# Optimization experiments

Hardware: AMD Instinct MI355X
Metric: run time of the kernel (lower is better)

Reference implementation:

```python
import jax, jax.numpy as jnp
import numpy as np

B, T, D, H = 4, 2048, 1024, 16
HD = D // H  # 64

def setup_inputs() -> dict:
    key = jax.random.key(0)
    ks = jax.random.split(key, 6)
    s = 0.02
    x = jax.random.normal(ks[0], (B, T, D), dtype=jnp.float32)
    # per-head projection weights, torch Linear layout [out=HD, in=D], stacked over heads
    Wq = jax.random.normal(ks[1], (H, HD, D), dtype=jnp.float32) * s
    Wk = jax.random.normal(ks[2], (H, HD, D), dtype=jnp.float32) * s
    Wv = jax.random.normal(ks[3], (H, HD, D), dtype=jnp.float32) * s
    Wo = jax.random.normal(ks[4], (D, D), dtype=jnp.float32) * s
    bo = jax.random.normal(ks[5], (D,), dtype=jnp.float32) * s
    return {"x": x, "Wq": Wq, "Wk": Wk, "Wv": Wv, "Wo": Wo, "bo": bo}

def reference(x, Wq, Wk, Wv, Wo, bo):
    # per-head projections (same math as per-head nn.Linear, vectorized over heads)
    Q = jnp.einsum('btd,hkd->bhtk', x, Wq)
    K = jnp.einsum('bsd,hkd->bhsk', x, Wk)
    V = jnp.einsum('bsd,hkd->bhsk', x, Wv)
    scale = 1.0 / jnp.sqrt(jnp.asarray(HD, x.dtype))
    logits = jnp.einsum('bhtk,bhsk->bhts', Q, K) * scale  # [B,H,T,S]
    w = jax.nn.softmax(logits, axis=-1)
    out = jnp.einsum('bhts,bhsk->bhtk', w, V)  # [B,H,T,HD]
    # concat heads in order -> [B,T,D]
    cat = jnp.transpose(out, (0, 2, 1, 3)).reshape(B, T, D)
    return cat @ Wo.T + bo
```

## Files before the change

kernel.cpp:

```cpp
#include <hip/hip_runtime.h>
#include <hip/hip_bf16.h>
#include <stdint.h>
#include <math.h>

typedef unsigned short u16;
typedef uint32_t u32;
typedef __bf16 bf16x8 __attribute__((ext_vector_type(8)));
typedef float f32x4 __attribute__((ext_vector_type(4)));
typedef float f32x16 __attribute__((ext_vector_type(16)));
typedef u16 u16x8 __attribute__((ext_vector_type(8)));
typedef u16 u16x4 __attribute__((ext_vector_type(4)));

#define B_ 4
#define T_ 2048
#define D_ 1024
#define H_ 16
#define HD_ 64
#define M_ (B_*T_)
#define LDA 72

__device__ __forceinline__ u16 f2bf(float f) {
    union { __bf16 h; u16 u; } c;
    c.h = (__bf16)f;
    return c.u;
}

__device__ __forceinline__ void gl16(const u16* g, u16* l) {
    __builtin_amdgcn_global_load_lds(
        (__attribute__((address_space(1))) void*)g,
        (__attribute__((address_space(3))) void*)l, 16, 0, 0);
}

__device__ __forceinline__ f32x4 mfma16(bf16x8 a, bf16x8 b, f32x4 c) {
    return __builtin_amdgcn_mfma_f32_16x16x32_bf16(a, b, c, 0, 0, 0);
}

__device__ __forceinline__ f32x16 mfma32(bf16x8 a, bf16x8 b, f32x16 c) {
    return __builtin_amdgcn_mfma_f32_32x32x16_bf16(a, b, c, 0, 0, 0);
}

__device__ __forceinline__ u32 cvtpk_bf16(float lo, float hi) {
    u32 r;
    asm("v_cvt_pk_bf16_f32 %0, %1, %2" : "=v"(r) : "v"(lo), "v"(hi));
    return r;
}

__device__ __forceinline__ float fexp2(float x) {
    return __builtin_amdgcn_exp2f(x);
}

__global__ __launch_bounds__(256) void precast(
    const float* __restrict__ x,  const float* __restrict__ wq,
    const float* __restrict__ wk, const float* __restrict__ wv,
    const float* __restrict__ wo,
    u16* __restrict__ xb, u16* __restrict__ wqb, u16* __restrict__ wkb,
    u16* __restrict__ wvb, u16* __restrict__ wob)
{
    const int which = blockIdx.y;
    const float* src; u16* dst; int n;
    switch (which) {
        case 0: src = x;  dst = xb;  n = M_ * D_;  break;
        case 1: src = wq; dst = wqb; n = D_ * D_;  break;
        case 2: src = wk; dst = wkb; n = D_ * D_;  break;
        case 3: src = wv; dst = wvb; n = D_ * D_;  break;
        default: src = wo; dst = wob; n = D_ * D_; break;
    }
    int i = (blockIdx.x * 256 + threadIdx.x) * 4;
    if (i >= n) return;
    float4 v = *(const float4*)&src[i];
    u16x4 p = { f2bf(v.x), f2bf(v.y), f2bf(v.z), f2bf(v.w) };
    *(u16x4*)&dst[i] = p;
}

__device__ __forceinline__ void gemm_pipe(
    const u16* __restrict__ Xg, const u16* __restrict__ Wg,
    u16* AsBase, u16* BsBase,
    const int tid, const int wm, const int wn, const int l15, const int quad,
    f32x4 acc[8][4])
{
    const int swz = (quad ^ ((l15 >> 1) & 3)) * 8;

#pragma unroll
    for (int tt = 0; tt < 2; ++tt) {
#pragma unroll
        for (int i = 0; i < 4; ++i) {
            int c = tid + i * 256;
            int r = c >> 2, xs = (c & 3) ^ ((r >> 1) & 3);
            gl16(Xg + (size_t)r * 1024 + tt * 32 + xs * 8, AsBase + tt * 8192 + c * 8);
        }
#pragma unroll
        for (int i = 0; i < 2; ++i) {
            int c = tid + i * 256;
            int r = c >> 2, xs = (c & 3) ^ ((r >> 1) & 3);
            gl16(Wg + (size_t)r * 1024 + tt * 32 + xs * 8, BsBase + tt * 4096 + c * 8);
        }
    }

    for (int t = 0; t < 32; ++t) {
        if (t < 31) asm volatile("s_waitcnt vmcnt(6)" ::: "memory");
        else        asm volatile("s_waitcnt vmcnt(0)" ::: "memory");
        __builtin_amdgcn_s_barrier();
        __builtin_amdgcn_sched_barrier(0);
        const u16* Ac = AsBase + (t & 1) * 8192;
        const u16* Bc = BsBase + (t & 1) * 4096;
        bf16x8 af[8], bfr[4];
#pragma unroll
        for (int mf = 0; mf < 8; ++mf)
            af[mf] = *(const bf16x8*)&Ac[(wm * 128 + mf * 16 + l15) * 32 + swz];
#pragma unroll
        for (int nf = 0; nf < 4; ++nf)
            bfr[nf] = *(const bf16x8*)&Bc[(wn * 64 + nf * 16 + l15) * 32 + swz];
        asm volatile("s_waitcnt lgkmcnt(0)" ::: "memory");
        __builtin_amdgcn_sched_barrier(0);
        __builtin_amdgcn_s_barrier();
        if (t + 2 < 32) {
            const int k0 = (t + 2) * 32;
#pragma unroll
            for (int i = 0; i < 4; ++i) {
                int c = tid + i * 256;
                int r = c >> 2, xs = (c & 3) ^ ((r >> 1) & 3);
                gl16(Xg + (size_t)r * 1024 + k0 + xs * 8, AsBase + (t & 1) * 8192 + c * 8);
            }
#pragma unroll
            for (int i = 0; i < 2; ++i) {
                int c = tid + i * 256;
                int r = c >> 2, xs = (c & 3) ^ ((r >> 1) & 3);
                gl16(Wg + (size_t)r * 1024 + k0 + xs * 8, BsBase + (t & 1) * 4096 + c * 8);
            }
        }
        __builtin_amdgcn_s_setprio(1);
#pragma unroll
        for (int mf = 0; mf < 8; ++mf)
#pragma unroll
            for (int nf = 0; nf < 4; ++nf)
                acc[mf][nf] = mfma16(af[mf], bfr[nf], acc[mf][nf]);
        __builtin_amdgcn_s_setprio(0);
    }
}

__global__ __launch_bounds__(256, 2) void qkv_gemm(
    const u16* __restrict__ Xb, const u16* __restrict__ W3,
    u16* __restrict__ Qo, u16* __restrict__ Ko, u16* __restrict__ Vo)
{
    __shared__ __attribute__((aligned(16))) u16 As[2][256 * 32];
    __shared__ __attribute__((aligned(16))) u16 Bs[2][128 * 32];

    const int wg = blockIdx.x + 24 * blockIdx.y;
    const int xcd = wg & 7, k = wg >> 3;
    const int by = xcd + 8 * (k / 24);
    const int bx = k % 24;
    const int n0 = bx * 128, m0 = by * 256;
    const u16* Xg = Xb + (size_t)m0 * 1024;
    const u16* Wg = W3 + (size_t)n0 * 1024;
    const int z = n0 >> 10;
    u16* Out = (z == 0) ? Qo : (z == 1) ? Ko : Vo;
    const float qs = (z == 0) ? 0.125f * 1.44269504088896340736f : 1.0f;

    const int tid = threadIdx.x;
    const int lane = tid & 63;
    const int wave = tid >> 6;
    const int wm = wave >> 1, wn = wave & 1;
    const int l15 = lane & 15, quad = lane >> 4;

    f32x4 acc[8][4];
#pragma unroll
    for (int i = 0; i < 8; ++i)
#pragma unroll
        for (int j = 0; j < 4; ++j) acc[i][j] = (f32x4){0.f, 0.f, 0.f, 0.f};

    gemm_pipe(Xg, Wg, &As[0][0], &Bs[0][0], tid, wm, wn, l15, quad, acc);

#pragma unroll
    for (int mf = 0; mf < 8; ++mf)
#pragma unroll
        for (int nf = 0; nf < 4; ++nf)
#pragma unroll
            for (int r = 0; r < 4; ++r) {
                int row = m0 + wm * 128 + mf * 16 + quad * 4 + r;
                int colz = (n0 & 1023) + wn * 64 + nf * 16 + l15;
                int b = row >> 11;
                int t = row & 2047;
                int h = colz >> 6;
                int hd = colz & 63;
                Out[((b * H_ + h) * T_ + t) * HD_ + hd] = f2bf(acc[mf][nf][r] * qs);
            }
}

__global__ __launch_bounds__(256, 2) void out_gemm(
    const u16* __restrict__ Xb, const u16* __restrict__ W3,
    const float* __restrict__ bias, float* __restrict__ Out)
{
    __shared__ __attribute__((aligned(16))) u16 As[2][256 * 32];
    __shared__ __attribute__((aligned(16))) u16 Bs[2][128 * 32];

    const int wg = blockIdx.x + 8 * blockIdx.y;
    const int xcd = wg & 7, k = wg >> 3;
    const int by = xcd + 8 * (k >> 3);
    const int bx = k & 7;
    const int n0 = bx * 128, m0 = by * 256;
    const u16* Xg = Xb + (size_t)m0 * 1024;
    const u16* Wg = W3 + (size_t)n0 * 1024;

    const int tid = threadIdx.x;
    const int lane = tid & 63;
    const int wave = tid >> 6;
    const int wm = wave >> 1, wn = wave & 1;
    const int l15 = lane & 15, quad = lane >> 4;

    f32x4 acc[8][4];
#pragma unroll
    for (int i = 0; i < 8; ++i)
#pragma unroll
        for (int j = 0; j < 4; ++j) acc[i][j] = (f32x4){0.f, 0.f, 0.f, 0.f};

    gemm_pipe(Xg, Wg, &As[0][0], &Bs[0][0], tid, wm, wn, l15, quad, acc);

#pragma unroll
    for (int mf = 0; mf < 8; ++mf)
#pragma unroll
        for (int nf = 0; nf < 4; ++nf)
#pragma unroll
            for (int r = 0; r < 4; ++r) {
                int row = m0 + wm * 128 + mf * 16 + quad * 4 + r;
                int col = n0 + wn * 64 + nf * 16 + l15;
                Out[(size_t)row * 1024 + col] = acc[mf][nf][r] + bias[col];
            }
}

__global__ __launch_bounds__(256) void vtrans(
    const u16* __restrict__ Vin, u16* __restrict__ Vout)
{
    __shared__ __attribute__((aligned(16))) u16 Tt[64 * LDA];
    const int tid = threadIdx.x;
    const int t0 = blockIdx.x * 64;
    const size_t base = (size_t)blockIdx.y * T_ * HD_;

#pragma unroll
    for (int i = 0; i < 2; ++i) {
        int ch = tid + i * 256;
        int r = ch >> 3, c = (ch & 7) * 8;
        u16x8 v = *(const u16x8*)&Vin[base + (size_t)(t0 + r) * HD_ + c];
#pragma unroll
        for (int j = 0; j < 8; ++j) {
            int hd = c + j;
            int blk = (r >> 3) ^ ((hd >> 3) & 7);
            Tt[hd * LDA + blk * 8 + (r & 7)] = v[j];
        }
    }
    __syncthreads();
#pragma unroll
    for (int i = 0; i < 2; ++i) {
        int ch = tid + i * 256;
        int hd = ch >> 3, n = ch & 7;
        int k = (hd >> 3) & 7;
        u16x8 v = *(const u16x8*)&Tt[hd * LDA + ((n ^ k) * 8)];
        *(u16x8*)&Vout[base + (size_t)hd * T_ + t0 + n * 8] = v;
    }
}

__global__ __launch_bounds__(256, 2) void attn(
    const u16* __restrict__ Q, const u16* __restrict__ K,
    const u16* __restrict__ Vt_g, u16* __restrict__ O)
{
    __shared__ __attribute__((aligned(16))) u16 Ks[2 * 4096];
    __shared__ __attribute__((aligned(16))) u16 Vts[2 * 4096];
    __shared__ float lps[4 * 64];

    const int tid = threadIdx.x;
    const int lane = tid & 63, w = tid >> 6;
    const int l31 = lane & 31, hi = lane >> 5;

    const int wg = blockIdx.x + (T_ / 256) * (blockIdx.y + H_ * blockIdx.z);
    const int xcd = wg & 7, k8 = wg >> 3;
    const int bh = xcd + 8 * (k8 >> 3);
    const int xq = k8 & 7;
    const int b = bh >> 4, h = bh & 15;
    const int t0 = xq * 256 + w * 64;

    const size_t base = (size_t)bh * T_ * HD_;
    const u16* Kb = K + base;
    const u16* Vtb = Vt_g + base;
    const u16* Qb = Q + base + (size_t)t0 * HD_;

    const int ca = tid,        ra = ca >> 3,  sa = (ca & 7) ^ (ra & 7);
    const int cb2 = tid + 256, rb = cb2 >> 3, sb = (cb2 & 7) ^ (rb & 7);
    const u16* kpa = Kb  + (size_t)ra * 64 + sa * 8;
    const u16* kpb = Kb  + (size_t)rb * 64 + sb * 8;
    const u16* vpa = Vtb + (size_t)ra * T_ + sa * 8;
    const u16* vpb = Vtb + (size_t)rb * T_ + sb * 8;

    int foff[2][4];
#pragma unroll
    for (int nt = 0; nt < 2; ++nt) {
        const int row = nt * 32 + l31;
#pragma unroll
        for (int kb = 0; kb < 4; ++kb)
            foff[nt][kb] = row * 64 + (((kb * 2 + hi) ^ (row & 7)) * 8);
    }

    bf16x8 qf[2][4];
#pragma unroll
    for (int qt = 0; qt < 2; ++qt)
#pragma unroll
        for (int kb = 0; kb < 4; ++kb)
            qf[qt][kb] = *(const bf16x8*)&Qb[(qt * 32 + l31) * 64 + kb * 16 + hi * 8];

    f32x16 zacc;
#pragma unroll
    for (int i = 0; i < 16; ++i) zacc[i] = 0.f;
    f32x16 oacc[2][2];
#pragma unroll
    for (int qt = 0; qt < 2; ++qt)
#pragma unroll
        for (int cb = 0; cb < 2; ++cb) oacc[qt][cb] = zacc;
    float lp[2] = {0.f, 0.f};

    gl16(kpa, &Ks[ca * 8]);
    gl16(kpb, &Ks[cb2 * 8]);
    gl16(vpa, &Vts[ca * 8]);
    gl16(vpb, &Vts[cb2 * 8]);
    asm volatile("s_waitcnt vmcnt(0)" ::: "memory");
    __syncthreads();

    int buf = 0;
    for (int s0 = 0; s0 < T_; s0 += 64) {
        if (s0 + 64 < T_) {
            const int nb = buf ^ 1;
            const size_t ko = (size_t)(s0 + 64) * 64;
            const size_t vo = (size_t)(s0 + 64);
            gl16(kpa + ko, &Ks[nb * 4096 + ca * 8]);
            gl16(kpb + ko, &Ks[nb * 4096 + cb2 * 8]);
            gl16(vpa + vo, &Vts[nb * 4096 + ca * 8]);
            gl16(vpb + vo, &Vts[nb * 4096 + cb2 * 8]);
        }
        const u16* Kc = &Ks[buf * 4096];
        const u16* Vc = &Vts[buf * 4096];

        bf16x8 pa[2][4];
#pragma unroll
        for (int nt = 0; nt < 2; ++nt) {
            bf16x8 kf[4];
#pragma unroll
            for (int kb = 0; kb < 4; ++kb)
                kf[kb] = *(const bf16x8*)&Kc[foff[nt][kb]];
#pragma unroll
            for (int qt = 0; qt < 2; ++qt) {
                __builtin_amdgcn_s_setprio(1);
                f32x16 sacc = mfma32(kf[0], qf[qt][0], zacc);
                sacc = mfma32(kf[1], qf[qt][1], sacc);
                sacc = mfma32(kf[2], qf[qt][2], sacc);
                sacc = mfma32(kf[3], qf[qt][3], sacc);
                __builtin_amdgcn_s_setprio(0);
                float p[16];
#pragma unroll
                for (int r = 0; r < 16; ++r) p[r] = fexp2(sacc[r]);
                float s01 = (p[0] + p[1]) + (p[2] + p[3]);
                float s23 = (p[4] + p[5]) + (p[6] + p[7]);
                float s45 = (p[8] + p[9]) + (p[10] + p[11]);
                float s67 = (p[12] + p[13]) + (p[14] + p[15]);
                lp[qt] += (s01 + s23) + (s45 + s67);
#pragma unroll
                for (int c = 0; c < 2; ++c) {
                    const int g = c * 8;
                    u32 a0 = cvtpk_bf16(p[g + 0], p[g + 1]);
                    u32 a1 = cvtpk_bf16(p[g + 2], p[g + 3]);
                    u32 b0 = cvtpk_bf16(p[g + 4], p[g + 5]);
                    u32 b1 = cvtpk_bf16(p[g + 6], p[g + 7]);
                    asm("v_permlane32_swap_b32 %0, %1" : "+v"(a0), "+v"(b0));
                    asm("v_permlane32_swap_b32 %0, %1" : "+v"(a1), "+v"(b1));
                    union { u32 wq[4]; bf16x8 v; } uu;
                    uu.wq[0] = a0; uu.wq[1] = a1; uu.wq[2] = b0; uu.wq[3] = b1;
                    pa[qt][nt * 2 + c] = uu.v;
                }
            }
        }
        __builtin_amdgcn_s_setprio(1);
#pragma unroll
        for (int cb = 0; cb < 2; ++cb)
#pragma unroll
            for (int kb = 0; kb < 4; ++kb) {
                bf16x8 vf = *(const bf16x8*)&Vc[foff[cb][kb]];
                oacc[0][cb] = mfma32(pa[0][kb], vf, oacc[0][cb]);
                oacc[1][cb] = mfma32(pa[1][kb], vf, oacc[1][cb]);
            }
        __builtin_amdgcn_s_setprio(0);
        asm volatile("s_waitcnt vmcnt(0)" ::: "memory");
        __syncthreads();
        buf ^= 1;
    }

#pragma unroll
    for (int qt = 0; qt < 2; ++qt) {
        lp[qt] += __shfl_xor(lp[qt], 32);
        lps[w * 64 + qt * 32 + l31] = lp[qt];
    }
    asm volatile("s_waitcnt lgkmcnt(0)" ::: "memory");

#pragma unroll
    for (int qt = 0; qt < 2; ++qt)
#pragma unroll
        for (int r = 0; r < 16; ++r) {
            const int trow = (r & 3) + 8 * (r >> 2) + 4 * hi;
            const float dn = 1.f / lps[w * 64 + qt * 32 + trow];
            const int t = t0 + qt * 32 + trow;
#pragma unroll
            for (int cb = 0; cb < 2; ++cb) {
                const int col = h * 64 + cb * 32 + l31;
                O[((size_t)b * T_ + t) * D_ + col] = f2bf(oacc[qt][cb][r] * dn);
            }
        }
}

extern "C" void kernel_launch(void* const* d_in, const int* in_sizes, int n_in,
                              void* d_out, int out_size, void* d_ws, size_t ws_size,
                              hipStream_t stream) {
    const float* x  = (const float*)d_in[0];
    const float* Wq = (const float*)d_in[1];
    const float* Wk = (const float*)d_in[2];
    const float* Wv = (const float*)d_in[3];
    const float* Wo = (const float*)d_in[4];
    const float* bo = (const float*)d_in[5];
    float* out = (float*)d_out;

    const size_t n_qkv = (size_t)B_ * H_ * T_ * HD_;
    const size_t n_w   = (size_t)D_ * D_;
    u16* Qw  = (u16*)d_ws;
    u16* Kw  = Qw + n_qkv;
    u16* Vw  = Kw + n_qkv;
    u16* Vtw = Vw + n_qkv;
    u16* Xb  = Vtw;
    u16* Wqb = Vtw + n_qkv;
    u16* Wkb = Wqb + n_w;
    u16* Wvb = Wkb + n_w;
    u16* Wob = Wvb + n_w;
    u16* Ow  = Vw;

    dim3 gc(8192, 5);
    precast<<<gc, 256, 0, stream>>>(x, Wq, Wk, Wv, Wo, Xb, Wqb, Wkb, Wvb, Wob);

    dim3 g1(3072 / 128, M_ / 256);
    qkv_gemm<<<g1, 256, 0, stream>>>(Xb, Wqb, Qw, Kw, Vw);

    dim3 gt(T_ / 64, B_ * H_);
    vtrans<<<gt, 256, 0, stream>>>(Vw, Vtw);

    dim3 g2(T_ / 256, H_, B_);
    attn<<<g2, 256, 0, stream>>>(Qw, Kw, Vtw, Ow);

    dim3 g3(1024 / 128, M_ / 256);
    out_gemm<<<g3, 256, 0, stream>>>(Ow, Wob, bo, out);
}
```

Baseline: 271.4 us.

## Restructure projection GEMMs to 8 waves with BK=64 triple-buffered LDS pipeline

Both projection GEMMs now run 512 threads (8 waves, each owning a 64x64 sub-tile) instead of 4 waves each owning 128x64. The K step grows from 32 to 64 with a three-stage LDS ring, an 8-way XOR swizzle and one barrier per iteration in place of two. The XCD-to-tile mapping also changes so each XCD handles contiguous row blocks. The aim is more latency hiding and fewer barriers, at the cost of 144KB of LDS per block, which likely limits occupancy to one block per CU despite the launch bound of 2.

```diff
diff --git a/kernel.cpp b/kernel.cpp
--- a/kernel.cpp
+++ b/kernel.cpp
@@ -72,82 +72,98 @@
     *(u16x4*)&dst[i] = p;
 }
 
-__device__ __forceinline__ void gemm_pipe(
+__device__ __forceinline__ void gemm8_pipe(
     const u16* __restrict__ Xg, const u16* __restrict__ Wg,
-    u16* AsBase, u16* BsBase,
+    u16* As, u16* Bs,
     const int tid, const int wm, const int wn, const int l15, const int quad,
-    f32x4 acc[8][4])
-{
-    const int swz = (quad ^ ((l15 >> 1) & 3)) * 8;
+    f32x4 acc[4][4])
+{
+    const u16* asrc[4]; int adst[4];
+#pragma unroll
+    for (int i = 0; i < 4; ++i) {
+        int c = tid + i * 512;
+        int row = c >> 3, slot = c & 7;
+        asrc[i] = Xg + (size_t)row * 1024 + (slot ^ (row & 7)) * 8;
+        adst[i] = c * 8;
+    }
+    const u16* bsrc[2]; int bdst[2];
+#pragma unroll
+    for (int i = 0; i < 2; ++i) {
+        int c = tid + i * 512;
+        int row = c >> 3, slot = c & 7;
+        bsrc[i] = Wg + (size_t)row * 1024 + (slot ^ (row & 7)) * 8;
+        bdst[i] = c * 8;
+    }
+    const int sw = l15 & 7;
+    const int so0 = (quad ^ sw) * 8;
+    const int so1 = ((4 + quad) ^ sw) * 8;
 
 #pragma unroll
     for (int tt = 0; tt < 2; ++tt) {
 #pragma unroll
-        for (int i = 0; i < 4; ++i) {
-            int c = tid + i * 256;
-            int r = c >> 2, xs = (c & 3) ^ ((r >> 1) & 3);
-            gl16(Xg + (size_t)r * 1024 + tt * 32 + xs * 8, AsBase + tt * 8192 + c * 8);
-        }
-#pragma unroll
-        for (int i = 0; i < 2; ++i) {
-            int c = tid + i * 256;
-            int r = c >> 2, xs = (c & 3) ^ ((r >> 1) & 3);
-            gl16(Wg + (size_t)r * 1024 + tt * 32 + xs * 8, BsBase + tt * 4096 + c * 8);
-        }
-    }
-
-    for (int t = 0; t < 32; ++t) {
-        if (t < 31) asm volatile("s_waitcnt vmcnt(6)" ::: "memory");
-        else        asm volatile("s_waitcnt vmcnt(0)" ::: "memory");
+        for (int i = 0; i < 4; ++i) gl16(asrc[i] + tt * 64, As + tt * 16384 + adst[i]);
+#pragma unroll
+        for (int i = 0; i < 2; ++i) gl16(bsrc[i] + tt * 64, Bs + tt * 8192 + bdst[i]);
+    }
+    asm volatile("s_waitcnt vmcnt(6)" ::: "memory");
+    __builtin_amdgcn_s_barrier();
+
+#pragma unroll
+    for (int t = 0; t < 16; ++t) {
+        const u16* Ab = As + (t % 3) * 16384;
+        const u16* Bb = Bs + (t % 3) * 8192;
+        if (t + 2 < 16) {
+            const int k2 = (t + 2) * 64;
+            u16* An = As + ((t + 2) % 3) * 16384;
+            u16* Bn = Bs + ((t + 2) % 3) * 8192;
+#pragma unroll
+            for (int i = 0; i < 4; ++i) gl16(asrc[i] + k2, An + adst[i]);
+#pragma unroll
+            for (int i = 0; i < 2; ++i) gl16(bsrc[i] + k2, Bn + bdst[i]);
+        }
+        __builtin_amdgcn_sched_barrier(0);
+        bf16x8 af0[4], af1[4], bf0[4], bf1[4];
+#pragma unroll
+        for (int mf = 0; mf < 4; ++mf) {
+            const int rr = (wm * 64 + mf * 16 + l15) * 64;
+            af0[mf] = *(const bf16x8*)&Ab[rr + so0];
+            af1[mf] = *(const bf16x8*)&Ab[rr + so1];
+        }
+#pragma unroll
+        for (int nf = 0; nf < 4; ++nf) {
+            const int rr = (wn * 64 + nf * 16 + l15) * 64;
+            bf0[nf] = *(const bf16x8*)&Bb[rr + so0];
+            bf1[nf] = *(const bf16x8*)&Bb[rr + so1];
+        }
+        __builtin_amdgcn_s_setprio(1);
+#pragma unroll
+        for (int mf = 0; mf < 4; ++mf)
+#pragma unroll
+            for (int nf = 0; nf < 4; ++nf)
+                acc[mf][nf] = mfma16(af0[mf], bf0[nf], acc[mf][nf]);
+#pragma unroll
+        for (int mf = 0; mf < 4; ++mf)
+#pragma unroll
+            for (int nf = 0; nf < 4; ++nf)
+                acc[mf][nf] = mfma16(af1[mf], bf1[nf], acc[mf][nf]);
+        __builtin_amdgcn_s_setprio(0);
+        __builtin_amdgcn_sched_barrier(0);
+        if (t + 2 < 16)      asm volatile("s_waitcnt vmcnt(6)" ::: "memory");
+        else if (t + 1 < 16) asm volatile("s_waitcnt vmcnt(0)" ::: "memory");
         __builtin_amdgcn_s_barrier();
-        __builtin_amdgcn_sched_barrier(0);
-        const u16* Ac = AsBase + (t & 1) * 8192;
-        const u16* Bc = BsBase + (t & 1) * 4096;
-        bf16x8 af[8], bfr[4];
-#pragma unroll
-        for (int mf = 0; mf < 8; ++mf)
-            af[mf] = *(const bf16x8*)&Ac[(wm * 128 + mf * 16 + l15) * 32 + swz];
-#pragma unroll
-        for (int nf = 0; nf < 4; ++nf)
-            bfr[nf] = *(const bf16x8*)&Bc[(wn * 64 + nf * 16 + l15) * 32 + swz];
-        asm volatile("s_waitcnt lgkmcnt(0)" ::: "memory");
-        __builtin_amdgcn_sched_barrier(0);
-        __builtin_amdgcn_s_barrier();
-        if (t + 2 < 32) {
-            const int k0 = (t + 2) * 32;
-#pragma unroll
-            for (int i = 0; i < 4; ++i) {
-                int c = tid + i * 256;
-                int r = c >> 2, xs = (c & 3) ^ ((r >> 1) & 3);
-                gl16(Xg + (size_t)r * 1024 + k0 + xs * 8, AsBase + (t & 1) * 8192 + c * 8);
-            }
-#pragma unroll
-            for (int i = 0; i < 2; ++i) {
-                int c = tid + i * 256;
-                int r = c >> 2, xs = (c & 3) ^ ((r >> 1) & 3);
-                gl16(Wg + (size_t)r * 1024 + k0 + xs * 8, BsBase + (t & 1) * 4096 + c * 8);
-            }
-        }
-        __builtin_amdgcn_s_setprio(1);
-#pragma unroll
-        for (int mf = 0; mf < 8; ++mf)
-#pragma unroll
-            for (int nf = 0; nf < 4; ++nf)
-                acc[mf][nf] = mfma16(af[mf], bfr[nf], acc[mf][nf]);
-        __builtin_amdgcn_s_setprio(0);
-    }
-}
-
-__global__ __launch_bounds__(256, 2) void qkv_gemm(
+    }
+}
+
+__global__ __launch_bounds__(512, 2) void qkv_gemm(
     const u16* __restrict__ Xb, const u16* __restrict__ W3,
     u16* __restrict__ Qo, u16* __restrict__ Ko, u16* __restrict__ Vo)
 {
-    __shared__ __attribute__((aligned(16))) u16 As[2][256 * 32];
-    __shared__ __attribute__((aligned(16))) u16 Bs[2][128 * 32];
+    __shared__ __attribute__((aligned(16))) u16 As[3 * 256 * 64];
+    __shared__ __attribute__((aligned(16))) u16 Bs[3 * 128 * 64];
 
     const int wg = blockIdx.x + 24 * blockIdx.y;
     const int xcd = wg & 7, k = wg >> 3;
-    const int by = xcd + 8 * (k / 24);
+    const int by = xcd * 4 + (k / 24);
     const int bx = k % 24;
     const int n0 = bx * 128, m0 = by * 256;
     const u16* Xg = Xb + (size_t)m0 * 1024;
@@ -162,21 +178,21 @@
     const int wm = wave >> 1, wn = wave & 1;
     const int l15 = lane & 15, quad = lane >> 4;
 
-    f32x4 acc[8][4];
-#pragma unroll
-    for (int i = 0; i < 8; ++i)
+    f32x4 acc[4][4];
+#pragma unroll
+    for (int i = 0; i < 4; ++i)
 #pragma unroll
         for (int j = 0; j < 4; ++j) acc[i][j] = (f32x4){0.f, 0.f, 0.f, 0.f};
 
-    gemm_pipe(Xg, Wg, &As[0][0], &Bs[0][0], tid, wm, wn, l15, quad, acc);
-
-#pragma unroll
-    for (int mf = 0; mf < 8; ++mf)
+    gemm8_pipe(Xg, Wg, &As[0], &Bs[0], tid, wm, wn, l15, quad, acc);
+
+#pragma unroll
+    for (int mf = 0; mf < 4; ++mf)
 #pragma unroll
         for (int nf = 0; nf < 4; ++nf)
 #pragma unroll
             for (int r = 0; r < 4; ++r) {
-                int row = m0 + wm * 128 + mf * 16 + quad * 4 + r;
+                int row = m0 + wm * 64 + mf * 16 + quad * 4 + r;
                 int colz = (n0 & 1023) + wn * 64 + nf * 16 + l15;
                 int b = row >> 11;
                 int t = row & 2047;
@@ -186,16 +202,16 @@
             }
 }
 
-__global__ __launch_bounds__(256, 2) void out_gemm(
+__global__ __launch_bounds__(512, 2) void out_gemm(
     const u16* __restrict__ Xb, const u16* __restrict__ W3,
     const float* __restrict__ bias, float* __restrict__ Out)
 {
-    __shared__ __attribute__((aligned(16))) u16 As[2][256 * 32];
-    __shared__ __attribute__((aligned(16))) u16 Bs[2][128 * 32];
+    __shared__ __attribute__((aligned(16))) u16 As[3 * 256 * 64];
+    __shared__ __attribute__((aligned(16))) u16 Bs[3 * 128 * 64];
 
     const int wg = blockIdx.x + 8 * blockIdx.y;
     const int xcd = wg & 7, k = wg >> 3;
-    const int by = xcd + 8 * (k >> 3);
+    const int by = xcd * 4 + (k / 8);
     const int bx = k & 7;
     const int n0 = bx * 128, m0 = by * 256;
     const u16* Xg = Xb + (size_t)m0 * 1024;
@@ -207,21 +223,21 @@
     const int wm = wave >> 1, wn = wave & 1;
     const int l15 = lane & 15, quad = lane >> 4;
 
-    f32x4 acc[8][4];
-#pragma unroll
-    for (int i = 0; i < 8; ++i)
+    f32x4 acc[4][4];
+#pragma unroll
+    for (int i = 0; i < 4; ++i)
 #pragma unroll
         for (int j = 0; j < 4; ++j) acc[i][j] = (f32x4){0.f, 0.f, 0.f, 0.f};
 
-    gemm_pipe(Xg, Wg, &As[0][0], &Bs[0][0], tid, wm, wn, l15, quad, acc);
-
-#pragma unroll
-    for (int mf = 0; mf < 8; ++mf)
+    gemm8_pipe(Xg, Wg, &As[0], &Bs[0], tid, wm, wn, l15, quad, acc);
+
+#pragma unroll
+    for (int mf = 0; mf < 4; ++mf)
 #pragma unroll
         for (int nf = 0; nf < 4; ++nf)
 #pragma unroll
             for (int r = 0; r < 4; ++r) {
-                int row = m0 + wm * 128 + mf * 16 + quad * 4 + r;
+                int row = m0 + wm * 64 + mf * 16 + quad * 4 + r;
                 int col = n0 + wn * 64 + nf * 16 + l15;
                 Out[(size_t)row * 1024 + col] = acc[mf][nf][r] + bias[col];
             }
@@ -439,7 +455,7 @@
     precast<<<gc, 256, 0, stream>>>(x, Wq, Wk, Wv, Wo, Xb, Wqb, Wkb, Wvb, Wob);
 
     dim3 g1(3072 / 128, M_ / 256);
-    qkv_gemm<<<g1, 256, 0, stream>>>(Xb, Wqb, Qw, Kw, Vw);
+    qkv_gemm<<<g1, 512, 0, stream>>>(Xb, Wqb, Qw, Kw, Vw);
 
     dim3 gt(T_ / 64, B_ * H_);
     vtrans<<<gt, 256, 0, stream>>>(Vw, Vtw);
@@ -448,5 +464,5 @@
     attn<<<g2, 256, 0, stream>>>(Qw, Kw, Vtw, Ow);
 
     dim3 g3(1024 / 128, M_ / 256);
-    out_gemm<<<g3, 256, 0, stream>>>(Ow, Wob, bo, out);
-}
+    out_gemm<<<g3, 512, 0, stream>>>(Ow, Wob, bo, out);
+}
```

New measurement: 268.5 us. About the same (-1.0%).
